# Kernel optimization log

Measured on AMD Instinct MI355X. Metric: run time of the kernel, lower is better.

The kernel has to match this reference:

```python
import jax, jax.numpy as jnp
import numpy as np

B, S, D = 4, 4096, 64


def setup_inputs() -> dict:
    key = jax.random.key(0)
    ks = jax.random.split(key, 11)
    std = 1.0 / np.sqrt(D)
    inp = {
        "q": jax.random.normal(ks[0], (B, S, D), jnp.float32),
        "k": jax.random.normal(ks[1], (B, S, D), jnp.float32),
        "v": jax.random.normal(ks[2], (B, S, D), jnp.float32),
        # torch.nn.Linear params: weight [out,in], bias [out]
        "Wq": jax.random.uniform(ks[3], (D, D), jnp.float32, -std, std),
        "bq": jax.random.uniform(ks[4], (D,), jnp.float32, -std, std),
        "Wk": jax.random.uniform(ks[5], (D, D), jnp.float32, -std, std),
        "bk": jax.random.uniform(ks[6], (D,), jnp.float32, -std, std),
        "Wv": jax.random.uniform(ks[7], (D, D), jnp.float32, -std, std),
        "bv": jax.random.uniform(ks[8], (D,), jnp.float32, -std, std),
        "Wp": jax.random.uniform(ks[9], (D, D), jnp.float32, -std, std),
        "bp": jax.random.uniform(ks[10], (D,), jnp.float32, -std, std),
    }
    return inp


def reference(q, k, v, Wq, bq, Wk, bk, Wv, bv, Wp, bp):
    Q = q @ Wq.T + bq                      # [B,S,D]
    K = k @ Wk.T + bk
    V = v @ Wv.T + bv
    scale = 1.0 / jnp.sqrt(jnp.asarray(Q.shape[-1], Q.dtype))
    s = jnp.einsum('bqd,bkd->bqk', Q, K) * scale   # [B,S,S]
    # faithful to torch.tril(full_like(-inf), diagonal=-1): -inf strictly below diagonal
    i = jnp.arange(S)[:, None]
    j = jnp.arange(S)[None, :]
    s = jnp.where(i > j, -jnp.inf, s)
    o = jax.nn.softmax(s, axis=-1) @ V             # [B,S,D]
    return o @ Wp.T + bp
```

## Files before the change

kernel.cpp:

```cpp
#include <hip/hip_runtime.h>
#include <hip/hip_bf16.h>

#define S_LEN 4096
#define D_DIM 64
#define NBATCH 4

typedef unsigned short u16;
typedef unsigned int u32;
typedef __attribute__((ext_vector_type(8))) __bf16 bf16x8;
typedef __attribute__((ext_vector_type(4))) float f32x4;
typedef __attribute__((ext_vector_type(16))) float f32x16;
typedef __attribute__((ext_vector_type(2))) unsigned uint2v;

__device__ __forceinline__ u16 f_to_bf16u(float f) {
    union { float f; u32 u; } x; x.f = f;
    u32 r = x.u + 0x7fffu + ((x.u >> 16) & 1u);
    return (u16)(r >> 16);
}

__device__ __forceinline__ u32 pack_bf16_2(float a, float b) {
    union { __hip_bfloat162 h; u32 u; } z;
    z.h = __float22bfloat162_rn(float2{a, b});
    return z.u;
}

__global__ __launch_bounds__(256, 2)
void proj_qkv_kernel(const float* __restrict__ q, const float* __restrict__ k,
                     const float* __restrict__ v,
                     const float* __restrict__ Wq, const float* __restrict__ bq,
                     const float* __restrict__ Wk, const float* __restrict__ bk,
                     const float* __restrict__ Wv, const float* __restrict__ bv,
                     u16* __restrict__ Qb, u16* __restrict__ Kb, u16* __restrict__ Vt)
{
    __shared__ __align__(16) u16 vt[64 * 72];

    const int p = blockIdx.y;
    const float* inp  = (p == 0) ? q  : (p == 1) ? k  : v;
    const float* W    = (p == 0) ? Wq : (p == 1) ? Wk : Wv;
    const float* bias = (p == 0) ? bq : (p == 1) ? bk : bv;
    const float scl   = (p == 0) ? 0.18033688011112042f : 1.0f;

    const int tid  = threadIdx.x;
    const int wid  = tid >> 6;
    const int lane = tid & 63;
    const int ln   = lane & 15;
    const int qd   = lane >> 4;
    const int row0 = blockIdx.x * 64;
    const int r0w  = row0 + wid * 16;

    bf16x8 afrag[2];
#pragma unroll
    for (int c = 0; c < 2; ++c) {
        const float* src = inp + (r0w + ln) * 64 + c * 32 + qd * 8;
        float4 f0 = *(const float4*)src;
        float4 f1 = *(const float4*)(src + 4);
        bf16x8 a;
        a[0] = (__bf16)f0.x; a[1] = (__bf16)f0.y; a[2] = (__bf16)f0.z; a[3] = (__bf16)f0.w;
        a[4] = (__bf16)f1.x; a[5] = (__bf16)f1.y; a[6] = (__bf16)f1.z; a[7] = (__bf16)f1.w;
        afrag[c] = a;
    }

    bf16x8 bfrag[4][2];
    float  bcol[4];
#pragma unroll
    for (int nb = 0; nb < 4; ++nb) {
        bcol[nb] = bias[nb * 16 + ln];
#pragma unroll
        for (int c = 0; c < 2; ++c) {
            const float* src = W + (nb * 16 + ln) * 64 + c * 32 + qd * 8;
            float4 f0 = *(const float4*)src;
            float4 f1 = *(const float4*)(src + 4);
            bf16x8 b;
            b[0] = (__bf16)f0.x; b[1] = (__bf16)f0.y; b[2] = (__bf16)f0.z; b[3] = (__bf16)f0.w;
            b[4] = (__bf16)f1.x; b[5] = (__bf16)f1.y; b[6] = (__bf16)f1.z; b[7] = (__bf16)f1.w;
            bfrag[nb][c] = b;
        }
    }

    f32x4 acc[4];
#pragma unroll
    for (int nb = 0; nb < 4; ++nb) acc[nb] = (f32x4){0.f, 0.f, 0.f, 0.f};
#pragma unroll
    for (int c = 0; c < 2; ++c)
#pragma unroll
        for (int nb = 0; nb < 4; ++nb)
            acc[nb] = __builtin_amdgcn_mfma_f32_16x16x32_bf16(afrag[c], bfrag[nb][c], acc[nb], 0, 0, 0);

    if (p < 2) {
        u16* dst = (p == 0) ? Qb : Kb;
#pragma unroll
        for (int nb = 0; nb < 4; ++nb)
#pragma unroll
            for (int r = 0; r < 4; ++r) {
                int row = r0w + qd * 4 + r;
                dst[row * 64 + nb * 16 + ln] = f_to_bf16u((acc[nb][r] + bcol[nb]) * scl);
            }
    } else {
#pragma unroll
        for (int nb = 0; nb < 4; ++nb)
#pragma unroll
            for (int r = 0; r < 4; ++r)
                vt[(wid * 16 + qd * 4 + r) * 72 + nb * 16 + ln] = f_to_bf16u(acc[nb][r] + bcol[nb]);
        __syncthreads();
        const int d  = tid >> 2;
        const int sc = tid & 3;
        const int b  = row0 >> 12;
        const int sb = row0 & 4095;
        __align__(16) u16 tmp[16];
#pragma unroll
        for (int i = 0; i < 16; ++i) tmp[i] = vt[(sc * 16 + i) * 72 + d];
        u16* dstp = Vt + (size_t)b * (64 * S_LEN) + d * S_LEN + sb + sc * 16;
        *(uint4*)(dstp)     = *(const uint4*)(tmp);
        *(uint4*)(dstp + 8) = *(const uint4*)(tmp + 8);
    }
}

#define KSTR 72
#define KTILE (64 * KSTR)

__global__ __launch_bounds__(256, 4)
void flash_kernel(const u16* __restrict__ Qb, const u16* __restrict__ Kb,
                  const u16* __restrict__ Vt, u16* __restrict__ Op,
                  float* __restrict__ Lp)
{
    __shared__ __align__(16) u16 kv[2][2 * KTILE];

    const int tid  = threadIdx.x;
    const int wid  = tid >> 6;
    const int lane = tid & 63;
    const int l31  = lane & 31;
    const int lh   = lane >> 5;

    const int bid   = blockIdx.x;
    const int batch = bid & 3;
    const int c     = (bid >> 2) & 15;
    const int p     = bid >> 6;

    const int  srow = tid >> 2;
    const int  sch0 = (tid & 3) * 2;
    const u16* kgp  = Kb + ((size_t)batch * S_LEN + srow) * 64 + sch0 * 8;
    const u16* vgp  = Vt + (size_t)batch * (64 * S_LEN) + (size_t)srow * S_LEN + sch0 * 8;

    int cur = 0;

    for (int ph = 0; ph < 2; ++ph) {
        const int band = ph ? (31 - p) : p;
        const int i0w  = band * 128 + wid * 32;
        const int jt0  = 2 * band + ((c - 2 * band) & 15);

        bf16x8 qf[4];
        {
            const u16* qb = Qb + ((size_t)batch * S_LEN + i0w + l31) * 64;
#pragma unroll
            for (int c2 = 0; c2 < 4; ++c2)
                qf[c2] = *(const bf16x8*)(qb + c2 * 16 + lh * 8);
        }

        f32x16 o0, o1;
#pragma unroll
        for (int r = 0; r < 16; ++r) { o0[r] = 0.f; o1[r] = 0.f; }
        float lsum = 0.f;

        if (jt0 < 64) {
            __syncthreads();
            {
                const int j0 = jt0 * 64;
                uint4 k0 = *(const uint4*)(kgp + (size_t)j0 * 64);
                uint4 k1 = *(const uint4*)(kgp + (size_t)j0 * 64 + 8);
                uint4 v0 = *(const uint4*)(vgp + j0);
                uint4 v1 = *(const uint4*)(vgp + j0 + 8);
                u16* kb = &kv[cur][srow * KSTR];
                *(uint4*)(kb + (sch0 + 0) * 8) = k0;
                *(uint4*)(kb + (sch0 + 1) * 8) = k1;
                u16* vb = &kv[cur][KTILE + srow * KSTR];
                *(uint4*)(vb + (sch0 + 0) * 8) = v0;
                *(uint4*)(vb + (sch0 + 1) * 8) = v1;
            }

            for (int jt = jt0; jt < 64; jt += 16) {
                __syncthreads();
                const bool more = (jt + 16) < 64;
                uint4 kp0, kp1, vp0, vp1;
                if (more) {
                    const int jn = (jt + 16) * 64;
                    kp0 = *(const uint4*)(kgp + (size_t)jn * 64);
                    kp1 = *(const uint4*)(kgp + (size_t)jn * 64 + 8);
                    vp0 = *(const uint4*)(vgp + jn);
                    vp1 = *(const uint4*)(vgp + jn + 8);
                }
                const u16* kb = &kv[cur][0];
                const u16* vb = &kv[cur][KTILE];
                const int j0 = jt * 64;
                const bool needmask = (j0 < i0w + 32);
                const int qr = i0w + l31 - j0;

#pragma unroll
                for (int mi = 0; mi < 2; ++mi) {
                    f32x16 s;
#pragma unroll
                    for (int r = 0; r < 16; ++r) s[r] = 0.f;
#pragma unroll
                    for (int c2 = 0; c2 < 4; ++c2) {
                        bf16x8 a = *(const bf16x8*)(kb + (mi * 32 + l31) * KSTR + c2 * 16 + lh * 8);
                        s = __builtin_amdgcn_mfma_f32_32x32x16_bf16(a, qf[c2], s, 0, 0, 0);
                    }

                    float pv[16];
#pragma unroll
                    for (int r = 0; r < 16; ++r) pv[r] = exp2f(s[r]);
                    if (needmask) {
#pragma unroll
                        for (int g = 0; g < 4; ++g)
#pragma unroll
                            for (int i = 0; i < 4; ++i) {
                                const int kcol = mi * 32 + g * 8 + 4 * lh + i;
                                if (kcol < qr) pv[g * 4 + i] = 0.f;
                            }
                    }
#pragma unroll
                    for (int r = 0; r < 16; ++r) lsum += pv[r];

                    u32 u[4][2];
#pragma unroll
                    for (int R = 0; R < 4; ++R) {
                        u[R][0] = pack_bf16_2(pv[4 * R + 0], pv[4 * R + 1]);
                        u[R][1] = pack_bf16_2(pv[4 * R + 2], pv[4 * R + 3]);
                    }
#pragma unroll
                    for (int c1 = 0; c1 < 2; ++c1) {
                        union { u32 w[4]; bf16x8 v; } pa;
#if __has_builtin(__builtin_amdgcn_permlane32_swap)
                        uint2v p02 = __builtin_amdgcn_permlane32_swap(u[2 * c1][0], u[2 * c1 + 1][0], false, false);
                        uint2v p13 = __builtin_amdgcn_permlane32_swap(u[2 * c1][1], u[2 * c1 + 1][1], false, false);
                        pa.w[0] = p02.x; pa.w[1] = p13.x;
                        pa.w[2] = p02.y; pa.w[3] = p13.y;
#else
                        const u32 x0 = lh ? u[2 * c1][0] : u[2 * c1 + 1][0];
                        const u32 x1 = lh ? u[2 * c1][1] : u[2 * c1 + 1][1];
                        const u32 xs0 = (u32)__shfl_xor((int)x0, 32);
                        const u32 xs1 = (u32)__shfl_xor((int)x1, 32);
                        pa.w[0] = lh ? xs0 : u[2 * c1][0];
                        pa.w[1] = lh ? xs1 : u[2 * c1][1];
                        pa.w[2] = lh ? u[2 * c1 + 1][0] : xs0;
                        pa.w[3] = lh ? u[2 * c1 + 1][1] : xs1;
#endif
                        const int c2 = mi * 2 + c1;
                        bf16x8 v0f = *(const bf16x8*)(vb + l31 * KSTR + c2 * 16 + lh * 8);
                        bf16x8 v1f = *(const bf16x8*)(vb + (32 + l31) * KSTR + c2 * 16 + lh * 8);
                        o0 = __builtin_amdgcn_mfma_f32_32x32x16_bf16(pa.v, v0f, o0, 0, 0, 0);
                        o1 = __builtin_amdgcn_mfma_f32_32x32x16_bf16(pa.v, v1f, o1, 0, 0, 0);
                    }
                }

                if (more) {
                    u16* kb2 = &kv[cur ^ 1][srow * KSTR];
                    *(uint4*)(kb2 + (sch0 + 0) * 8) = kp0;
                    *(uint4*)(kb2 + (sch0 + 1) * 8) = kp1;
                    u16* vb2 = &kv[cur ^ 1][KTILE + srow * KSTR];
                    *(uint4*)(vb2 + (sch0 + 0) * 8) = vp0;
                    *(uint4*)(vb2 + (sch0 + 1) * 8) = vp1;
                }
                cur ^= 1;
            }
        }

        const int slot = (batch * 32 + band) * 16 + c;
        u16* ob = Op + (size_t)slot * 8192;
#pragma unroll
        for (int r = 0; r < 16; ++r) {
            const int qrl = (r & 3) + 8 * (r >> 2) + 4 * lh;
            ob[(wid * 32 + qrl) * 64 + l31]      = f_to_bf16u(o0[r]);
            ob[(wid * 32 + qrl) * 64 + 32 + l31] = f_to_bf16u(o1[r]);
        }
        lsum += __shfl_xor(lsum, 32);
        if (lh == 0) Lp[(size_t)slot * 128 + wid * 32 + l31] = lsum;
    }
}

__global__ __launch_bounds__(256, 2)
void combine_proj_kernel(const u16* __restrict__ Op, const float* __restrict__ Lp,
                         const float* __restrict__ Wp, const float* __restrict__ bp,
                         float* __restrict__ out)
{
    const int tid  = threadIdx.x;
    const int wid  = tid >> 6;
    const int lane = tid & 63;
    const int ln   = lane & 15;
    const int qd   = lane >> 4;
    const int g    = blockIdx.x * 64 + wid * 16;
    const int row  = g + ln;

    const int batch = row >> 12;
    const int sr    = row & 4095;
    const int band  = sr >> 7;
    const int rl    = sr & 127;
    const int sbase = (batch * 32 + band) * 16;

    float acc0[8], acc1[8];
#pragma unroll
    for (int j = 0; j < 8; ++j) { acc0[j] = 0.f; acc1[j] = 0.f; }
    float l = 0.f;
#pragma unroll
    for (int s = 0; s < 16; ++s) {
        const int slot = sbase + s;
        const u16* op = Op + (size_t)slot * 8192 + rl * 64 + qd * 8;
        bf16x8 x0 = *(const bf16x8*)op;
        bf16x8 x1 = *(const bf16x8*)(op + 32);
#pragma unroll
        for (int j = 0; j < 8; ++j) { acc0[j] += (float)x0[j]; acc1[j] += (float)x1[j]; }
        l += Lp[(size_t)slot * 128 + rl];
    }
    float inv = 1.0f / l;
    bf16x8 afrag[2];
#pragma unroll
    for (int j = 0; j < 8; ++j) { afrag[0][j] = (__bf16)(acc0[j] * inv); afrag[1][j] = (__bf16)(acc1[j] * inv); }

    bf16x8 bfrag[4][2];
    float  bcol[4];
#pragma unroll
    for (int nb = 0; nb < 4; ++nb) {
        bcol[nb] = bp[nb * 16 + ln];
#pragma unroll
        for (int cc = 0; cc < 2; ++cc) {
            const float* src = Wp + (nb * 16 + ln) * 64 + cc * 32 + qd * 8;
            float4 f0 = *(const float4*)src;
            float4 f1 = *(const float4*)(src + 4);
            bf16x8 b;
            b[0] = (__bf16)f0.x; b[1] = (__bf16)f0.y; b[2] = (__bf16)f0.z; b[3] = (__bf16)f0.w;
            b[4] = (__bf16)f1.x; b[5] = (__bf16)f1.y; b[6] = (__bf16)f1.z; b[7] = (__bf16)f1.w;
            bfrag[nb][cc] = b;
        }
    }

    f32x4 acc[4];
#pragma unroll
    for (int nb = 0; nb < 4; ++nb) acc[nb] = (f32x4){0.f, 0.f, 0.f, 0.f};
#pragma unroll
    for (int cc = 0; cc < 2; ++cc)
#pragma unroll
        for (int nb = 0; nb < 4; ++nb)
            acc[nb] = __builtin_amdgcn_mfma_f32_16x16x32_bf16(afrag[cc], bfrag[nb][cc], acc[nb], 0, 0, 0);

#pragma unroll
    for (int nb = 0; nb < 4; ++nb)
#pragma unroll
        for (int r = 0; r < 4; ++r) {
            int rowo = g + qd * 4 + r;
            out[(size_t)rowo * 64 + nb * 16 + ln] = acc[nb][r] + bcol[nb];
        }
}

extern "C" void kernel_launch(void* const* d_in, const int* in_sizes, int n_in,
                              void* d_out, int out_size, void* d_ws, size_t ws_size,
                              hipStream_t stream) {
    const float* q  = (const float*)d_in[0];
    const float* k  = (const float*)d_in[1];
    const float* v  = (const float*)d_in[2];
    const float* Wq = (const float*)d_in[3];
    const float* bq = (const float*)d_in[4];
    const float* Wk = (const float*)d_in[5];
    const float* bk = (const float*)d_in[6];
    const float* Wv = (const float*)d_in[7];
    const float* bv = (const float*)d_in[8];
    const float* Wp = (const float*)d_in[9];
    const float* bp = (const float*)d_in[10];
    float* out = (float*)d_out;

    const size_t NTOK = (size_t)NBATCH * S_LEN * D_DIM;
    u16* Qb = (u16*)d_ws;
    u16* Kb = Qb + NTOK;
    u16* Vt = Kb + NTOK;
    u16* Op = Vt + NTOK;
    float* Lp = (float*)(Op + (size_t)2048 * 8192);

    proj_qkv_kernel<<<dim3(256, 3), 256, 0, stream>>>(q, k, v, Wq, bq, Wk, bk, Wv, bv, Qb, Kb, Vt);
    flash_kernel<<<1024, 256, 0, stream>>>(Qb, Kb, Vt, Op, Lp);
    combine_proj_kernel<<<256, 256, 0, stream>>>(Op, Lp, Wp, bp, out);
}
```

Measured before the change: 123.6 us.

## Widen flash KV tile to 128 and split keys across waves with LDS reduction

```diff
diff --git a/kernel.cpp b/kernel.cpp
--- a/kernel.cpp
+++ b/kernel.cpp
@@ -116,164 +116,220 @@
 }
 
 #define KSTR 72
-#define KTILE (64 * KSTR)
-
-__global__ __launch_bounds__(256, 4)
+#define VSTR 136
+#define KVSZ (128 * KSTR + 64 * VSTR)
+
+__global__ __launch_bounds__(256, 2)
 void flash_kernel(const u16* __restrict__ Qb, const u16* __restrict__ Kb,
                   const u16* __restrict__ Vt, u16* __restrict__ Op,
                   float* __restrict__ Lp)
 {
-    __shared__ __align__(16) u16 kv[2][2 * KTILE];
+    __shared__ __align__(16) u16 kv[2][KVSZ];
 
     const int tid  = threadIdx.x;
     const int wid  = tid >> 6;
     const int lane = tid & 63;
     const int l31  = lane & 31;
     const int lh   = lane >> 5;
+    const int qh   = wid & 1;
+    const int kh   = wid >> 1;
 
     const int bid   = blockIdx.x;
     const int batch = bid & 3;
-    const int c     = (bid >> 2) & 15;
-    const int p     = bid >> 6;
-
-    const int  srow = tid >> 2;
-    const int  sch0 = (tid & 3) * 2;
+    const int c     = (bid >> 2) & 7;
+    const int pr    = bid >> 5;
+
+    const int  srow = tid >> 1;
+    const int  sch0 = (tid & 1) * 4;
+    const int  vrow = tid >> 2;
+    const int  vch0 = (tid & 3) * 4;
     const u16* kgp  = Kb + ((size_t)batch * S_LEN + srow) * 64 + sch0 * 8;
-    const u16* vgp  = Vt + (size_t)batch * (64 * S_LEN) + (size_t)srow * S_LEN + sch0 * 8;
+    const u16* vgp  = Vt + (size_t)batch * (64 * S_LEN) + (size_t)vrow * S_LEN + vch0 * 8;
 
     int cur = 0;
 
     for (int ph = 0; ph < 2; ++ph) {
-        const int band = ph ? (31 - p) : p;
-        const int i0w  = band * 128 + wid * 32;
-        const int jt0  = 2 * band + ((c - 2 * band) & 15);
-
-        bf16x8 qf[4];
-        {
-            const u16* qb = Qb + ((size_t)batch * S_LEN + i0w + l31) * 64;
-#pragma unroll
-            for (int c2 = 0; c2 < 4; ++c2)
-                qf[c2] = *(const bf16x8*)(qb + c2 * 16 + lh * 8);
-        }
-
-        f32x16 o0, o1;
-#pragma unroll
-        for (int r = 0; r < 16; ++r) { o0[r] = 0.f; o1[r] = 0.f; }
-        float lsum = 0.f;
-
-        if (jt0 < 64) {
+        const int band = ph ? (31 - pr) : pr;
+        const int jt0  = band + ((c - band) & 7);
+
+        f32x16 o[2][2];
+#pragma unroll
+        for (int qs = 0; qs < 2; ++qs)
+#pragma unroll
+            for (int ni = 0; ni < 2; ++ni)
+#pragma unroll
+                for (int r = 0; r < 16; ++r) o[qs][ni][r] = 0.f;
+        float ls[2] = {0.f, 0.f};
+
+        if (jt0 < 32) {
+            bf16x8 qf[2][4];
+#pragma unroll
+            for (int qs = 0; qs < 2; ++qs) {
+                const u16* qb = Qb + ((size_t)batch * S_LEN + band * 128 + qh * 64 + qs * 32 + l31) * 64;
+#pragma unroll
+                for (int c2 = 0; c2 < 4; ++c2)
+                    qf[qs][c2] = *(const bf16x8*)(qb + c2 * 16 + lh * 8);
+            }
+
             __syncthreads();
             {
-                const int j0 = jt0 * 64;
-                uint4 k0 = *(const uint4*)(kgp + (size_t)j0 * 64);
-                uint4 k1 = *(const uint4*)(kgp + (size_t)j0 * 64 + 8);
-                uint4 v0 = *(const uint4*)(vgp + j0);
-                uint4 v1 = *(const uint4*)(vgp + j0 + 8);
+                const int j0 = jt0 * 128;
+                uint4 kp[4], vp[4];
+#pragma unroll
+                for (int i = 0; i < 4; ++i) kp[i] = *(const uint4*)(kgp + (size_t)j0 * 64 + i * 8);
+#pragma unroll
+                for (int i = 0; i < 4; ++i) vp[i] = *(const uint4*)(vgp + j0 + i * 8);
                 u16* kb = &kv[cur][srow * KSTR];
-                *(uint4*)(kb + (sch0 + 0) * 8) = k0;
-                *(uint4*)(kb + (sch0 + 1) * 8) = k1;
-                u16* vb = &kv[cur][KTILE + srow * KSTR];
-                *(uint4*)(vb + (sch0 + 0) * 8) = v0;
-                *(uint4*)(vb + (sch0 + 1) * 8) = v1;
-            }
-
-            for (int jt = jt0; jt < 64; jt += 16) {
+#pragma unroll
+                for (int i = 0; i < 4; ++i) *(uint4*)(kb + (sch0 + i) * 8) = kp[i];
+                u16* vb = &kv[cur][128 * KSTR + vrow * VSTR];
+#pragma unroll
+                for (int i = 0; i < 4; ++i) *(uint4*)(vb + (vch0 + i) * 8) = vp[i];
+            }
+
+            for (int jt = jt0; jt < 32; jt += 8) {
                 __syncthreads();
-                const bool more = (jt + 16) < 64;
-                uint4 kp0, kp1, vp0, vp1;
+                const bool more = (jt + 8) < 32;
+                uint4 kp[4], vp[4];
                 if (more) {
-                    const int jn = (jt + 16) * 64;
-                    kp0 = *(const uint4*)(kgp + (size_t)jn * 64);
-                    kp1 = *(const uint4*)(kgp + (size_t)jn * 64 + 8);
-                    vp0 = *(const uint4*)(vgp + jn);
-                    vp1 = *(const uint4*)(vgp + jn + 8);
+                    const int jn = (jt + 8) * 128;
+#pragma unroll
+                    for (int i = 0; i < 4; ++i) kp[i] = *(const uint4*)(kgp + (size_t)jn * 64 + i * 8);
+#pragma unroll
+                    for (int i = 0; i < 4; ++i) vp[i] = *(const uint4*)(vgp + jn + i * 8);
                 }
                 const u16* kb = &kv[cur][0];
-                const u16* vb = &kv[cur][KTILE];
-                const int j0 = jt * 64;
-                const bool needmask = (j0 < i0w + 32);
-                const int qr = i0w + l31 - j0;
+                const u16* vb = &kv[cur][128 * KSTR];
+                const bool dm = (jt == band) && (kh <= qh);
 
 #pragma unroll
                 for (int mi = 0; mi < 2; ++mi) {
-                    f32x16 s;
-#pragma unroll
-                    for (int r = 0; r < 16; ++r) s[r] = 0.f;
-#pragma unroll
-                    for (int c2 = 0; c2 < 4; ++c2) {
-                        bf16x8 a = *(const bf16x8*)(kb + (mi * 32 + l31) * KSTR + c2 * 16 + lh * 8);
-                        s = __builtin_amdgcn_mfma_f32_32x32x16_bf16(a, qf[c2], s, 0, 0, 0);
+                    bf16x8 kf[4];
+#pragma unroll
+                    for (int c2 = 0; c2 < 4; ++c2)
+                        kf[c2] = *(const bf16x8*)(kb + (kh * 64 + mi * 32 + l31) * KSTR + c2 * 16 + lh * 8);
+
+                    bf16x8 pa[2][2];
+#pragma unroll
+                    for (int qs = 0; qs < 2; ++qs) {
+                        f32x16 s;
+#pragma unroll
+                        for (int r = 0; r < 16; ++r) s[r] = 0.f;
+#pragma unroll
+                        for (int c2 = 0; c2 < 4; ++c2)
+                            s = __builtin_amdgcn_mfma_f32_32x32x16_bf16(kf[c2], qf[qs][c2], s, 0, 0, 0);
+
+                        float pv[16];
+#pragma unroll
+                        for (int r = 0; r < 16; ++r) pv[r] = exp2f(s[r]);
+                        if (dm) {
+                            const int qrel = qh * 64 + qs * 32 + l31 - kh * 64;
+#pragma unroll
+                            for (int g = 0; g < 4; ++g)
+#pragma unroll
+                                for (int i = 0; i < 4; ++i) {
+                                    const int kc = mi * 32 + g * 8 + 4 * lh + i;
+                                    if (kc < qrel) pv[g * 4 + i] = 0.f;
+                                }
+                        }
+                        float la = 0.f;
+#pragma unroll
+                        for (int r = 0; r < 16; ++r) la += pv[r];
+                        ls[qs] += la;
+
+                        u32 u[4][2];
+#pragma unroll
+                        for (int R = 0; R < 4; ++R) {
+                            u[R][0] = pack_bf16_2(pv[4 * R + 0], pv[4 * R + 1]);
+                            u[R][1] = pack_bf16_2(pv[4 * R + 2], pv[4 * R + 3]);
+                        }
+#pragma unroll
+                        for (int c1 = 0; c1 < 2; ++c1) {
+                            union { u32 w[4]; bf16x8 v; } pp;
+#if __has_builtin(__builtin_amdgcn_permlane32_swap)
+                            uint2v p02 = __builtin_amdgcn_permlane32_swap(u[2 * c1][0], u[2 * c1 + 1][0], false, false);
+                            uint2v p13 = __builtin_amdgcn_permlane32_swap(u[2 * c1][1], u[2 * c1 + 1][1], false, false);
+                            pp.w[0] = p02.x; pp.w[1] = p13.x;
+                            pp.w[2] = p02.y; pp.w[3] = p13.y;
+#else
+                            const u32 x0 = lh ? u[2 * c1][0] : u[2 * c1 + 1][0];
+                            const u32 x1 = lh ? u[2 * c1][1] : u[2 * c1 + 1][1];
+                            const u32 xs0 = (u32)__shfl_xor((int)x0, 32);
+                            const u32 xs1 = (u32)__shfl_xor((int)x1, 32);
+                            pp.w[0] = lh ? xs0 : u[2 * c1][0];
+                            pp.w[1] = lh ? xs1 : u[2 * c1][1];
+                            pp.w[2] = lh ? u[2 * c1 + 1][0] : xs0;
+                            pp.w[3] = lh ? u[2 * c1 + 1][1] : xs1;
+#endif
+                            pa[qs][c1] = pp.v;
+                        }
                     }
 
-                    float pv[16];
-#pragma unroll
-                    for (int r = 0; r < 16; ++r) pv[r] = exp2f(s[r]);
-                    if (needmask) {
-#pragma unroll
-                        for (int g = 0; g < 4; ++g)
-#pragma unroll
-                            for (int i = 0; i < 4; ++i) {
-                                const int kcol = mi * 32 + g * 8 + 4 * lh + i;
-                                if (kcol < qr) pv[g * 4 + i] = 0.f;
-                            }
-                    }
-#pragma unroll
-                    for (int r = 0; r < 16; ++r) lsum += pv[r];
-
-                    u32 u[4][2];
-#pragma unroll
-                    for (int R = 0; R < 4; ++R) {
-                        u[R][0] = pack_bf16_2(pv[4 * R + 0], pv[4 * R + 1]);
-                        u[R][1] = pack_bf16_2(pv[4 * R + 2], pv[4 * R + 3]);
-                    }
 #pragma unroll
                     for (int c1 = 0; c1 < 2; ++c1) {
-                        union { u32 w[4]; bf16x8 v; } pa;
-#if __has_builtin(__builtin_amdgcn_permlane32_swap)
-                        uint2v p02 = __builtin_amdgcn_permlane32_swap(u[2 * c1][0], u[2 * c1 + 1][0], false, false);
-                        uint2v p13 = __builtin_amdgcn_permlane32_swap(u[2 * c1][1], u[2 * c1 + 1][1], false, false);
-                        pa.w[0] = p02.x; pa.w[1] = p13.x;
-                        pa.w[2] = p02.y; pa.w[3] = p13.y;
-#else
-                        const u32 x0 = lh ? u[2 * c1][0] : u[2 * c1 + 1][0];
-                        const u32 x1 = lh ? u[2 * c1][1] : u[2 * c1 + 1][1];
-                        const u32 xs0 = (u32)__shfl_xor((int)x0, 32);
-                        const u32 xs1 = (u32)__shfl_xor((int)x1, 32);
-                        pa.w[0] = lh ? xs0 : u[2 * c1][0];
-                        pa.w[1] = lh ? xs1 : u[2 * c1][1];
-                        pa.w[2] = lh ? u[2 * c1 + 1][0] : xs0;
-                        pa.w[3] = lh ? u[2 * c1 + 1][1] : xs1;
-#endif
-                        const int c2 = mi * 2 + c1;
-                        bf16x8 v0f = *(const bf16x8*)(vb + l31 * KSTR + c2 * 16 + lh * 8);
-                        bf16x8 v1f = *(const bf16x8*)(vb + (32 + l31) * KSTR + c2 * 16 + lh * 8);
-                        o0 = __builtin_amdgcn_mfma_f32_32x32x16_bf16(pa.v, v0f, o0, 0, 0, 0);
-                        o1 = __builtin_amdgcn_mfma_f32_32x32x16_bf16(pa.v, v1f, o1, 0, 0, 0);
+                        const int kofs = kh * 64 + (mi * 2 + c1) * 16 + lh * 8;
+                        bf16x8 v0f = *(const bf16x8*)(vb + l31 * VSTR + kofs);
+                        bf16x8 v1f = *(const bf16x8*)(vb + (32 + l31) * VSTR + kofs);
+#pragma unroll
+                        for (int qs = 0; qs < 2; ++qs) {
+                            o[qs][0] = __builtin_amdgcn_mfma_f32_32x32x16_bf16(pa[qs][c1], v0f, o[qs][0], 0, 0, 0);
+                            o[qs][1] = __builtin_amdgcn_mfma_f32_32x32x16_bf16(pa[qs][c1], v1f, o[qs][1], 0, 0, 0);
+                        }
                     }
                 }
 
                 if (more) {
                     u16* kb2 = &kv[cur ^ 1][srow * KSTR];
-                    *(uint4*)(kb2 + (sch0 + 0) * 8) = kp0;
-                    *(uint4*)(kb2 + (sch0 + 1) * 8) = kp1;
-                    u16* vb2 = &kv[cur ^ 1][KTILE + srow * KSTR];
-                    *(uint4*)(vb2 + (sch0 + 0) * 8) = vp0;
-                    *(uint4*)(vb2 + (sch0 + 1) * 8) = vp1;
+#pragma unroll
+                    for (int i = 0; i < 4; ++i) *(uint4*)(kb2 + (sch0 + i) * 8) = kp[i];
+                    u16* vb2 = &kv[cur ^ 1][128 * KSTR + vrow * VSTR];
+#pragma unroll
+                    for (int i = 0; i < 4; ++i) *(uint4*)(vb2 + (vch0 + i) * 8) = vp[i];
                 }
                 cur ^= 1;
             }
         }
 
-        const int slot = (batch * 32 + band) * 16 + c;
-        u16* ob = Op + (size_t)slot * 8192;
-#pragma unroll
-        for (int r = 0; r < 16; ++r) {
-            const int qrl = (r & 3) + 8 * (r >> 2) + 4 * lh;
-            ob[(wid * 32 + qrl) * 64 + l31]      = f_to_bf16u(o0[r]);
-            ob[(wid * 32 + qrl) * 64 + 32 + l31] = f_to_bf16u(o1[r]);
-        }
-        lsum += __shfl_xor(lsum, 32);
-        if (lh == 0) Lp[(size_t)slot * 128 + wid * 32 + l31] = lsum;
+        float* mb = (float*)&kv[0][0];
+        float* lb = mb + 2 * 64 * 68;
+        ls[0] += __shfl_xor(ls[0], 32);
+        ls[1] += __shfl_xor(ls[1], 32);
+
+        __syncthreads();
+        if (kh == 1) {
+#pragma unroll
+            for (int qs = 0; qs < 2; ++qs)
+#pragma unroll
+                for (int ni = 0; ni < 2; ++ni)
+#pragma unroll
+                    for (int r = 0; r < 16; ++r) {
+                        const int row = qh * 64 + qs * 32 + (r & 3) + 8 * (r >> 2) + 4 * lh;
+                        mb[row * 68 + ni * 32 + l31] = o[qs][ni][r];
+                    }
+            if (lh == 0) {
+                lb[qh * 64 + l31]      = ls[0];
+                lb[qh * 64 + 32 + l31] = ls[1];
+            }
+        }
+        __syncthreads();
+        if (kh == 0) {
+            const int slot = (batch * 32 + band) * 8 + c;
+            u16* ob = Op + (size_t)slot * 8192;
+#pragma unroll
+            for (int qs = 0; qs < 2; ++qs)
+#pragma unroll
+                for (int ni = 0; ni < 2; ++ni)
+#pragma unroll
+                    for (int r = 0; r < 16; ++r) {
+                        const int row = qh * 64 + qs * 32 + (r & 3) + 8 * (r >> 2) + 4 * lh;
+                        const float vsum = o[qs][ni][r] + mb[row * 68 + ni * 32 + l31];
+                        ob[row * 64 + ni * 32 + l31] = f_to_bf16u(vsum);
+                    }
+            if (lh == 0) {
+                Lp[(size_t)slot * 128 + qh * 64 + l31]      = ls[0] + lb[qh * 64 + l31];
+                Lp[(size_t)slot * 128 + qh * 64 + 32 + l31] = ls[1] + lb[qh * 64 + 32 + l31];
+            }
+        }
     }
 }
 
@@ -294,14 +350,14 @@
     const int sr    = row & 4095;
     const int band  = sr >> 7;
     const int rl    = sr & 127;
-    const int sbase = (batch * 32 + band) * 16;
+    const int sbase = (batch * 32 + band) * 8;
 
     float acc0[8], acc1[8];
 #pragma unroll
     for (int j = 0; j < 8; ++j) { acc0[j] = 0.f; acc1[j] = 0.f; }
     float l = 0.f;
 #pragma unroll
-    for (int s = 0; s < 16; ++s) {
+    for (int s = 0; s < 8; ++s) {
         const int slot = sbase + s;
         const u16* op = Op + (size_t)slot * 8192 + rl * 64 + qd * 8;
         bf16x8 x0 = *(const bf16x8*)op;
@@ -371,9 +427,9 @@
     u16* Kb = Qb + NTOK;
     u16* Vt = Kb + NTOK;
     u16* Op = Vt + NTOK;
-    float* Lp = (float*)(Op + (size_t)2048 * 8192);
+    float* Lp = (float*)(Op + (size_t)1024 * 8192);
 
     proj_qkv_kernel<<<dim3(256, 3), 256, 0, stream>>>(q, k, v, Wq, bq, Wk, bk, Wv, bv, Qb, Kb, Vt);
-    flash_kernel<<<1024, 256, 0, stream>>>(Qb, Kb, Vt, Op, Lp);
+    flash_kernel<<<512, 256, 0, stream>>>(Qb, Kb, Vt, Op, Lp);
     combine_proj_kernel<<<256, 256, 0, stream>>>(Op, Lp, Wp, bp, out);
 }
```

Result: slower. 140.9 us (+14.0%).
